# Kernel tuning notes

Measured on AMD Instinct MI355X. Metric: run time of the kernel, lower is better.

The kernel has to match this reference:

```python
import jax, jax.numpy as jnp
import numpy as np

D_MODEL = 1024
N_HEAD = 16
D_K = D_MODEL // N_HEAD
B, S = 2, 2048


def setup_inputs() -> dict:
    key = jax.random.key(0)
    ks = jax.random.split(key, 12)
    sc = 1.0 / np.sqrt(D_MODEL)
    return {
        "q": jax.random.normal(ks[0], (B, S, D_MODEL), jnp.float32),
        "k": jax.random.normal(ks[1], (B, S, D_MODEL), jnp.float32),
        "v": jax.random.normal(ks[2], (B, S, D_MODEL), jnp.float32),
        "mask": jax.random.randint(ks[3], (B, S, S), 0, 2, jnp.int32),
        # learned params (torch Linear convention: y = x @ W + b with W pre-transposed)
        "wq": jax.random.normal(ks[4], (D_MODEL, D_MODEL), jnp.float32) * sc,
        "bq": jax.random.normal(ks[5], (D_MODEL,), jnp.float32) * sc,
        "wk": jax.random.normal(ks[6], (D_MODEL, D_MODEL), jnp.float32) * sc,  # no bias
        "wv": jax.random.normal(ks[7], (D_MODEL, D_MODEL), jnp.float32) * sc,
        "bv": jax.random.normal(ks[8], (D_MODEL,), jnp.float32) * sc,
        "wf": jax.random.normal(ks[9], (D_MODEL, D_MODEL), jnp.float32) * sc,
        "bf": jax.random.normal(ks[10], (D_MODEL,), jnp.float32) * sc,
    }


def reference(q, k, v, mask, wq, bq, wk, wv, bv, wf, bf):
    bs = q.shape[0]
    temperature = jnp.asarray(D_K ** 0.5, q.dtype)
    # projections -> [b, h, s, d_k]
    qh = (q @ wq + bq).reshape(bs, -1, N_HEAD, D_K).transpose(0, 2, 1, 3)
    kh = (k @ wk).reshape(bs, -1, N_HEAD, D_K).transpose(0, 2, 1, 3)
    vh = (v @ wv + bv).reshape(bs, -1, N_HEAD, D_K).transpose(0, 2, 1, 3)
    # scores [b, h, sq, sk]
    attn = jnp.einsum("bhqd,bhkd->bhqk", qh, kh) / temperature
    m0 = (mask[:, None, :, :] == 0)  # mask==0 -> masked out, broadcast over heads
    attn = jnp.where(m0, -jnp.inf, attn)
    attn = jax.nn.softmax(attn, axis=-1)
    attn = jnp.where(m0, 0.0, attn)
    out = jnp.einsum("bhqk,bhkd->bhqd", attn, vh)
    out = out.transpose(0, 2, 1, 3).reshape(bs, -1, D_MODEL)
    return out @ wf + bf  # dropout is identity in eval mode
```

## Files before the change

### kernel.cpp

```cpp
#include <hip/hip_runtime.h>

#define D_MODEL 1024
#define NHEAD   16
#define DK      64
#define BATCH   2
#define SEQ     2048

typedef __attribute__((ext_vector_type(8))) short bf16x8;
typedef __attribute__((ext_vector_type(4))) short bf16x4;
typedef __attribute__((ext_vector_type(4))) float f32x4;
typedef __attribute__((ext_vector_type(2))) int i32x2;

#define QSCALE 0.18033688011f

__device__ __forceinline__ unsigned short f2b(float x) {
  unsigned u = __builtin_bit_cast(unsigned, x);
  u = (u + 0x7fffu + ((u >> 16) & 1u)) >> 16;
  return (unsigned short)u;
}
__device__ __forceinline__ unsigned short f2b_rhu(float x) {
  return (unsigned short)((__builtin_bit_cast(unsigned, x) + 0x8000u) >> 16);
}
__device__ __forceinline__ int pk2(float a, float b) {
  unsigned ua = __builtin_bit_cast(unsigned, a) + 0x8000u;
  unsigned ub = __builtin_bit_cast(unsigned, b) + 0x8000u;
  return (int)__builtin_amdgcn_perm(ub, ua, 0x07060302u);
}
__device__ __forceinline__ int pk2u(unsigned ua, unsigned ub) {
  return (int)__builtin_amdgcn_perm(ub + 0x8000u, ua + 0x8000u, 0x07060302u);
}

typedef const __attribute__((address_space(1))) void* gas_p;
typedef __attribute__((address_space(3))) void* las_p;
__device__ __forceinline__ void gll16(const void* g, void* l) {
  __builtin_amdgcn_global_load_lds((gas_p)g, (las_p)l, 16, 0, 0);
}

__device__ __forceinline__ f32x4 mfma16(bf16x4 a, bf16x4 b, f32x4 c) {
#if __has_builtin(__builtin_amdgcn_mfma_f32_16x16x16bf16_1k)
  return __builtin_amdgcn_mfma_f32_16x16x16bf16_1k(a, b, c, 0, 0, 0);
#else
  f32x4 d;
  asm("v_mfma_f32_16x16x16_bf16 %0, %1, %2, %3" : "=v"(d) : "v"(a), "v"(b), "v"(c));
  return d;
#endif
}

__global__ __launch_bounds__(256) void cast3_kernel(
    const float* __restrict__ q, const float* __restrict__ k, const float* __restrict__ v,
    unsigned short* __restrict__ qb, unsigned short* __restrict__ kb,
    unsigned short* __restrict__ vb) {
  const float* src = blockIdx.y == 0 ? q : (blockIdx.y == 1 ? k : v);
  unsigned short* dst = blockIdx.y == 0 ? qb : (blockIdx.y == 1 ? kb : vb);
  size_t i = ((size_t)blockIdx.x * 256 + threadIdx.x) * 8;
  float4 x0 = *(const float4*)&src[i];
  float4 x1 = *(const float4*)&src[i + 4];
  int4 w;
  w.x = pk2(x0.x, x0.y); w.y = pk2(x0.z, x0.w);
  w.z = pk2(x1.x, x1.y); w.w = pk2(x1.z, x1.w);
  *(int4*)&dst[i] = w;
}

__global__ __launch_bounds__(256) void wtrans_kernel(
    const float* __restrict__ wq, const float* __restrict__ wk,
    const float* __restrict__ wv, const float* __restrict__ wf,
    unsigned short* __restrict__ wqt, unsigned short* __restrict__ wkt,
    unsigned short* __restrict__ wvt, unsigned short* __restrict__ wft) {
  __shared__ float tile[64][65];
  const float* w; unsigned short* wt;
  switch (blockIdx.z) {
    case 0: w = wq; wt = wqt; break;
    case 1: w = wk; wt = wkt; break;
    case 2: w = wv; wt = wvt; break;
    default: w = wf; wt = wft; break;
  }
  int r0 = blockIdx.y * 64, c0 = blockIdx.x * 64;
  int t = threadIdx.x;
  for (int i = 0; i < 16; ++i) {
    int idx = t + i * 256; int r = idx >> 6, c = idx & 63;
    tile[r][c] = w[(size_t)(r0 + r) * D_MODEL + c0 + c];
  }
  __syncthreads();
  for (int i = 0; i < 16; ++i) {
    int idx = t + i * 256; int r = idx >> 6, c = idx & 63;
    wt[(size_t)(c0 + r) * D_MODEL + r0 + c] = f2b(tile[c][r]);
  }
}

__global__ __launch_bounds__(256) void maskpack_kernel(
    const int* __restrict__ mask, unsigned long long* __restrict__ mbits) {
  size_t gw = ((size_t)blockIdx.x * 256 + threadIdx.x) >> 6;
  int lane = threadIdx.x & 63;
  int val = mask[gw * 64 + lane];
  unsigned long long bits = __ballot(val != 0);
  if (lane == 0) mbits[gw] = bits;
}

__global__ __launch_bounds__(256) void gemm_qkv_kernel(
    const unsigned short* __restrict__ qb, const unsigned short* __restrict__ kb,
    const unsigned short* __restrict__ vb,
    const unsigned short* __restrict__ wqt, const unsigned short* __restrict__ wkt,
    const unsigned short* __restrict__ wvt,
    const float* __restrict__ bq, const float* __restrict__ bv,
    unsigned short* __restrict__ qh, unsigned short* __restrict__ kh,
    unsigned short* __restrict__ vt) {
  __shared__ unsigned short SB[16640];
  int bid = blockIdx.x;
  int xcd = bid & 7, slot = bid >> 3;
  int mi = slot & 3, zn = slot >> 2;
  int z = zn >> 3;
  int n0 = (zn & 7) * 128;
  int m0 = (mi * 8 + xcd) * 128;
  const unsigned short* A; const unsigned short* Bt;
  switch (z) {
    case 0:  A = qb; Bt = wqt; break;
    case 1:  A = kb; Bt = wkt; break;
    default: A = vb; Bt = wvt; break;
  }
  int t = threadIdx.x, lane = t & 63, wave = t >> 6;
  int l16 = lane & 15, quad = lane >> 4;
  int wm = (wave & 1) * 64, wn = (wave >> 1) * 64;
  f32x4 zero = {0.f, 0.f, 0.f, 0.f};
  f32x4 acc[4][4];
  for (int mt = 0; mt < 4; ++mt) for (int nt = 0; nt < 4; ++nt) acc[mt][nt] = zero;

  int drow = lane >> 2, dcol = (lane & 3) * 8;
  const unsigned short* asrc = A  + (size_t)(m0 + wave * 32 + drow) * D_MODEL + dcol;
  const unsigned short* bsrc = Bt + (size_t)(n0 + wave * 32 + drow) * D_MODEL + dcol;
  int dst = wave * 1024 + lane * 8;

#pragma unroll
  for (int g = 0; g < 2; ++g) {
    gll16(asrc + (size_t)(g * 16) * D_MODEL, &SB[dst + g * 512]);
    gll16(bsrc + (size_t)(g * 16) * D_MODEL, &SB[4096 + dst + g * 512]);
  }
  for (int it = 0; it < 32; ++it) {
    __syncthreads();
    if (it + 1 < 32) {
      int nb = ((it + 1) & 1) * 8192, kn = (it + 1) * 32;
#pragma unroll
      for (int g = 0; g < 2; ++g) {
        gll16(asrc + (size_t)(g * 16) * D_MODEL + kn, &SB[nb + dst + g * 512]);
        gll16(bsrc + (size_t)(g * 16) * D_MODEL + kn, &SB[nb + 4096 + dst + g * 512]);
      }
    }
    int cb = (it & 1) * 8192;
    bf16x8 a[4], b[4];
    for (int mt = 0; mt < 4; ++mt)
      a[mt] = *(const bf16x8*)&SB[cb + (wm + mt * 16 + l16) * 32 + quad * 8];
    for (int nt = 0; nt < 4; ++nt)
      b[nt] = *(const bf16x8*)&SB[cb + 4096 + (wn + nt * 16 + l16) * 32 + quad * 8];
    for (int mt = 0; mt < 4; ++mt)
      for (int nt = 0; nt < 4; ++nt)
        acc[mt][nt] = __builtin_amdgcn_mfma_f32_16x16x32_bf16(a[mt], b[nt], acc[mt][nt], 0, 0, 0);
  }

  if (z == 2) {
    __syncthreads();
#pragma unroll
    for (int nt = 0; nt < 4; ++nt) {
      int col = wn + nt * 16 + l16;
      float bb = bv[n0 + col];
      for (int mt = 0; mt < 4; ++mt)
        for (int r = 0; r < 4; ++r)
          SB[col * 130 + wm + mt * 16 + quad * 4 + r] = f2b_rhu(acc[mt][nt][r] + bb);
    }
    __syncthreads();
    int c = t >> 1, hf = t & 1;
    int colg = n0 + c, hh = colg >> 6, dd = colg & 63;
    int b_ = m0 >> 11, sbase = m0 & (SEQ - 1);
    unsigned short* dstp = vt + (((size_t)(b_ * NHEAD + hh)) * DK + dd) * SEQ + sbase + hf * 64;
#pragma unroll
    for (int j = 0; j < 8; ++j)
      *(int4*)(dstp + j * 8) = *(const int4*)&SB[c * 130 + hf * 64 + j * 8];
  } else if (z == 0) {
    for (int nt = 0; nt < 4; ++nt) {
      int col = n0 + wn + nt * 16 + l16;
      float bb = bq[col];
      int h = col >> 6, d = col & 63;
      for (int mt = 0; mt < 4; ++mt)
        for (int r = 0; r < 4; ++r) {
          int row = m0 + wm + mt * 16 + quad * 4 + r;
          int b_ = row >> 11, s = row & (SEQ - 1);
          qh[(((size_t)(b_ * NHEAD + h) * SEQ) + s) * DK + d] =
              f2b_rhu((acc[mt][nt][r] + bb) * QSCALE);
        }
    }
  } else {
    for (int nt = 0; nt < 4; ++nt) {
      int col = n0 + wn + nt * 16 + l16;
      int h = col >> 6, d = col & 63;
      for (int mt = 0; mt < 4; ++mt)
        for (int r = 0; r < 4; ++r) {
          int row = m0 + wm + mt * 16 + quad * 4 + r;
          int b_ = row >> 11, s = row & (SEQ - 1);
          kh[(((size_t)(b_ * NHEAD + h) * SEQ) + s) * DK + d] = f2b_rhu(acc[mt][nt][r]);
        }
    }
  }
}

__global__ __launch_bounds__(256) void gemm_out_kernel(
    const unsigned short* __restrict__ A, const unsigned short* __restrict__ Bt,
    const float* __restrict__ bias, float* __restrict__ out) {
  __shared__ unsigned short As[8192], Bs[8192];
  int bid = blockIdx.x;
  int xcd = bid & 7, slot = bid >> 3;
  int mi = slot & 7, n0 = (slot >> 3) * 64;
  int m0 = (mi * 8 + xcd) * 64;
  int t = threadIdx.x, lane = t & 63, wave = t >> 6;
  int l16 = lane & 15, quad = lane >> 4;
  int wm = (wave & 1) * 32, wn = (wave >> 1) * 32;
  f32x4 zero = {0.f, 0.f, 0.f, 0.f};
  f32x4 acc[2][2];
  for (int mt = 0; mt < 2; ++mt) for (int nt = 0; nt < 2; ++nt) acc[mt][nt] = zero;

  int drow = lane >> 2, dcol = (lane & 3) * 8;
  const unsigned short* asrc = A  + (size_t)(m0 + wave * 16 + drow) * D_MODEL + dcol;
  const unsigned short* bsrc = Bt + (size_t)(n0 + wave * 16 + drow) * D_MODEL + dcol;
  int dst = wave * 512 + lane * 8;

#pragma unroll
  for (int hf = 0; hf < 2; ++hf) {
    gll16(asrc + hf * 32, &As[dst + hf * 2048]);
    gll16(bsrc + hf * 32, &Bs[dst + hf * 2048]);
  }
  for (int it = 0; it < 16; ++it) {
    __syncthreads();
    if (it + 1 < 16) {
      int nb = ((it + 1) & 1) * 4096, kn = (it + 1) * 64;
#pragma unroll
      for (int hf = 0; hf < 2; ++hf) {
        gll16(asrc + kn + hf * 32, &As[nb + dst + hf * 2048]);
        gll16(bsrc + kn + hf * 32, &Bs[nb + dst + hf * 2048]);
      }
    }
    int cb = (it & 1) * 4096;
#pragma unroll
    for (int half = 0; half < 2; ++half) {
      bf16x8 a[2], b[2];
      for (int mt = 0; mt < 2; ++mt)
        a[mt] = *(const bf16x8*)&As[cb + half * 2048 + (wm + mt * 16 + l16) * 32 + quad * 8];
      for (int nt = 0; nt < 2; ++nt)
        b[nt] = *(const bf16x8*)&Bs[cb + half * 2048 + (wn + nt * 16 + l16) * 32 + quad * 8];
      for (int mt = 0; mt < 2; ++mt)
        for (int nt = 0; nt < 2; ++nt)
          acc[mt][nt] = __builtin_amdgcn_mfma_f32_16x16x32_bf16(a[mt], b[nt], acc[mt][nt], 0, 0, 0);
    }
  }
  for (int nt = 0; nt < 2; ++nt) {
    int col = n0 + wn + nt * 16 + l16;
    float bb = bias[col];
    for (int mt = 0; mt < 2; ++mt)
      for (int r = 0; r < 4; ++r) {
        int row = m0 + wm + mt * 16 + quad * 4 + r;
        out[(size_t)row * D_MODEL + col] = acc[mt][nt][r] + bb;
      }
  }
}

__global__ __launch_bounds__(256, 2) void attn_kernel(
    const unsigned short* __restrict__ qh, const unsigned short* __restrict__ kh,
    const unsigned short* __restrict__ vt, const unsigned long long* __restrict__ mbits,
    unsigned short* __restrict__ attb) {
  __shared__ unsigned short Ks[8192];
  __shared__ unsigned short Vs[8192];
  int bid = blockIdx.x;
  int xcd = bid & 7, slot = bid >> 3;
  int bh_ = 4 * xcd + (slot >> 4);
  int qt = slot & 15;
  int b = bh_ >> 4, h = bh_ & 15;
  int t = threadIdx.x, lane = t & 63, wave = t >> 6;
  int l16 = lane & 15, quad = lane >> 4;
  size_t bh = (size_t)b * NHEAD + h;

  const unsigned short* Kg = kh + bh * SEQ * DK;
  const unsigned short* Vg = vt + bh * DK * SEQ;
  const unsigned long long* mrow = mbits + (size_t)b * SEQ * (SEQ / 64);

  bf16x8 qf[2][2];
#pragma unroll
  for (int qm = 0; qm < 2; ++qm) {
    const unsigned short* Qg =
        qh + (bh * SEQ + (size_t)(qt * 128 + wave * 32 + qm * 16 + l16)) * DK;
    qf[qm][0] = *(const bf16x8*)&Qg[quad * 8];
    qf[qm][1] = *(const bf16x8*)&Qg[32 + quad * 8];
  }

  int srow = lane >> 3;
  int schk = ((lane & 7) ^ (srow & 7)) * 8;
  const unsigned short* ks0 = Kg + (size_t)(wave * 16 + srow) * DK + schk;
  const unsigned short* ks1 = Kg + (size_t)(wave * 16 + 8 + srow) * DK + schk;
  const unsigned short* vs0 = Vg + (size_t)(wave * 16 + srow) * SEQ + schk;
  const unsigned short* vs1 = Vg + (size_t)(wave * 16 + 8 + srow) * SEQ + schk;
  int sdst = wave * 1024 + lane * 8;

  int x7 = l16 & 7;
  int ka0 = l16 * 64 + ((quad ^ x7) * 8);
  int ka1 = l16 * 64 + (((4 + quad) ^ x7) * 8);
  int va[4];
#pragma unroll
  for (int nt = 0; nt < 4; ++nt)
    va[nt] = l16 * 64 + (((nt * 2 + (quad >> 1)) ^ x7) * 8) + (quad & 1) * 4;

  bf16x4 ones4;
#pragma unroll
  for (int i = 0; i < 4; ++i) ones4[i] = (short)0x3F80;

  f32x4 zero = {0.f, 0.f, 0.f, 0.f};
  f32x4 accO[2][4], accRS[2];
#pragma unroll
  for (int qm = 0; qm < 2; ++qm) {
    accRS[qm] = zero;
    for (int dt = 0; dt < 4; ++dt) accO[qm][dt] = zero;
  }

  gll16(ks0, &Ks[sdst]);       gll16(ks1, &Ks[sdst + 512]);
  gll16(vs0, &Vs[sdst]);       gll16(vs1, &Vs[sdst + 512]);

  for (int tk = 0; tk < SEQ / 64; ++tk) {
    __syncthreads();
    if (tk + 1 < SEQ / 64) {
      int nb = ((tk + 1) & 1) * 4096;
      size_t ko = (size_t)(tk + 1) * 64 * DK;
      int vo = (tk + 1) * 64;
      gll16(ks0 + ko, &Ks[nb + sdst]);  gll16(ks1 + ko, &Ks[nb + sdst + 512]);
      gll16(vs0 + vo, &Vs[nb + sdst]);  gll16(vs1 + vo, &Vs[nb + sdst + 512]);
    }
    int cb = (tk & 1) * 4096;

    f32x4 accS[2][4];
#pragma unroll
    for (int qm = 0; qm < 2; ++qm)
      for (int nt = 0; nt < 4; ++nt) accS[qm][nt] = zero;
#pragma unroll
    for (int step = 0; step < 2; ++step) {
      int ka = step ? ka1 : ka0;
#pragma unroll
      for (int nt = 0; nt < 4; ++nt) {
        bf16x8 kf = *(const bf16x8*)&Ks[cb + ka + nt * 1024];
        accS[0][nt] = __builtin_amdgcn_mfma_f32_16x16x32_bf16(kf, qf[0][step], accS[0][nt], 0, 0, 0);
        accS[1][nt] = __builtin_amdgcn_mfma_f32_16x16x32_bf16(kf, qf[1][step], accS[1][nt], 0, 0, 0);
      }
    }

    bf16x4 ap[2][4];
#pragma unroll
    for (int qm = 0; qm < 2; ++qm) {
      int qrow = qt * 128 + wave * 32 + qm * 16 + l16;
      unsigned long long mq = mrow[(size_t)qrow * (SEQ / 64) + tk] >> (quad * 4);
      unsigned mlo = (unsigned)mq, mhi = (unsigned)(mq >> 32);
#pragma unroll
      for (int nt = 0; nt < 4; ++nt) {
        unsigned w = (nt < 2) ? mlo : mhi;
        unsigned pu[4];
#pragma unroll
        for (int r = 0; r < 4; ++r) {
          float pv = __builtin_amdgcn_exp2f(accS[qm][nt][r]);
          int msk = ((int)(w << (31 - ((nt & 1) * 16 + r)))) >> 31;
          pu[r] = __builtin_bit_cast(unsigned, pv) & (unsigned)msk;
        }
        i32x2 wv;
        wv[0] = pk2u(pu[0], pu[1]);
        wv[1] = pk2u(pu[2], pu[3]);
        ap[qm][nt] = __builtin_bit_cast(bf16x4, wv);
      }
#pragma unroll
      for (int nt = 0; nt < 4; ++nt)
        accRS[qm] = mfma16(ap[qm][nt], ones4, accRS[qm]);
    }

#pragma unroll
    for (int nt = 0; nt < 4; ++nt) {
      int vb_ = cb + va[nt];
#pragma unroll
      for (int dt = 0; dt < 4; ++dt) {
        bf16x4 vf = *(const bf16x4*)&Vs[vb_ + dt * 1024];
        accO[0][dt] = mfma16(ap[0][nt], vf, accO[0][dt]);
        accO[1][dt] = mfma16(ap[1][nt], vf, accO[1][dt]);
      }
    }
  }

#pragma unroll
  for (int qm = 0; qm < 2; ++qm)
    for (int r = 0; r < 4; ++r) {
      float sden = accRS[qm][r];
      float inv = sden > 0.f ? 1.f / sden : 0.f;
      int row = qt * 128 + wave * 32 + qm * 16 + quad * 4 + r;
      size_t ob = ((size_t)b * SEQ + row) * D_MODEL + (size_t)h * DK;
      for (int dt = 0; dt < 4; ++dt)
        attb[ob + dt * 16 + l16] = f2b_rhu(accO[qm][dt][r] * inv);
    }
}

extern "C" void kernel_launch(void* const* d_in, const int* in_sizes, int n_in,
                              void* d_out, int out_size, void* d_ws, size_t ws_size,
                              hipStream_t stream) {
  (void)in_sizes; (void)n_in; (void)out_size; (void)ws_size;
  const float* q    = (const float*)d_in[0];
  const float* k    = (const float*)d_in[1];
  const float* v    = (const float*)d_in[2];
  const int*   mask = (const int*)d_in[3];
  const float* wq   = (const float*)d_in[4];
  const float* bq   = (const float*)d_in[5];
  const float* wk   = (const float*)d_in[6];
  const float* wv   = (const float*)d_in[7];
  const float* bv   = (const float*)d_in[8];
  const float* wf   = (const float*)d_in[9];
  const float* bf   = (const float*)d_in[10];

  char* ws = (char*)d_ws;
  unsigned short* wft  = (unsigned short*)(ws + 0);
  unsigned short* wqt  = (unsigned short*)(ws + 2097152);
  unsigned short* wkt  = (unsigned short*)(ws + 4194304);
  unsigned short* wvt  = (unsigned short*)(ws + 6291456);
  unsigned short* attb = (unsigned short*)(ws + 2097152);
  unsigned short* qhp  = (unsigned short*)(ws + 10485760);
  unsigned short* khp  = (unsigned short*)(ws + 18874368);
  unsigned short* vtp  = (unsigned short*)(ws + 27262976);
  unsigned long long* mbits = (unsigned long long*)(ws + 35651584);
  unsigned short* vb   = (unsigned short*)(ws + 36700160);
  unsigned short* qb   = (unsigned short*)d_out;
  unsigned short* kb   = (unsigned short*)d_out + 4194304;

  hipLaunchKernelGGL(cast3_kernel, dim3(2048, 3), dim3(256), 0, stream, q, k, v, qb, kb, vb);
  hipLaunchKernelGGL(wtrans_kernel, dim3(16, 16, 4), dim3(256), 0, stream,
                     wq, wk, wv, wf, wqt, wkt, wvt, wft);
  hipLaunchKernelGGL(maskpack_kernel, dim3(32768), dim3(256), 0, stream, mask, mbits);
  hipLaunchKernelGGL(gemm_qkv_kernel, dim3(768), dim3(256), 0, stream,
                     qb, kb, vb, wqt, wkt, wvt, bq, bv, qhp, khp, vtp);
  hipLaunchKernelGGL(attn_kernel, dim3(512), dim3(256), 0, stream,
                     qhp, khp, vtp, mbits, attb);
  hipLaunchKernelGGL(gemm_out_kernel, dim3(1024), dim3(256), 0, stream,
                     attb, wft, bf, (float*)d_out);
}
```

Measured before the change: 280.3 us.

## Merge prep kernels, stage Q/K stores through LDS, shrink attention blocks

Folds the three preprocessing kernels (input cast, weight transpose, mask bit-packing) into one launch dispatched by block index, and mask packing now handles four 64-wide words per wave. The Q/K projection epilogue writes through shared memory so global stores become 16-byte coalesced rows instead of scattered 2-byte writes. The attention kernel moves to 128-thread blocks covering 64 query rows, doubling the grid to 1024 blocks, and each wave now loads four K/V chunks. Mask words are fetched early in the loop. The aims are fewer launches, better store coalescing and more attention parallelism, at the cost of less K/V tile reuse per block.

```diff
diff --git a/kernel.cpp b/kernel.cpp
--- a/kernel.cpp
+++ b/kernel.cpp
@@ -46,54 +46,61 @@
 #endif
 }
 
-__global__ __launch_bounds__(256) void cast3_kernel(
+__global__ __launch_bounds__(256) void prep_kernel(
     const float* __restrict__ q, const float* __restrict__ k, const float* __restrict__ v,
     unsigned short* __restrict__ qb, unsigned short* __restrict__ kb,
-    unsigned short* __restrict__ vb) {
-  const float* src = blockIdx.y == 0 ? q : (blockIdx.y == 1 ? k : v);
-  unsigned short* dst = blockIdx.y == 0 ? qb : (blockIdx.y == 1 ? kb : vb);
-  size_t i = ((size_t)blockIdx.x * 256 + threadIdx.x) * 8;
-  float4 x0 = *(const float4*)&src[i];
-  float4 x1 = *(const float4*)&src[i + 4];
-  int4 w;
-  w.x = pk2(x0.x, x0.y); w.y = pk2(x0.z, x0.w);
-  w.z = pk2(x1.x, x1.y); w.w = pk2(x1.z, x1.w);
-  *(int4*)&dst[i] = w;
-}
-
-__global__ __launch_bounds__(256) void wtrans_kernel(
+    unsigned short* __restrict__ vb,
     const float* __restrict__ wq, const float* __restrict__ wk,
     const float* __restrict__ wv, const float* __restrict__ wf,
     unsigned short* __restrict__ wqt, unsigned short* __restrict__ wkt,
-    unsigned short* __restrict__ wvt, unsigned short* __restrict__ wft) {
-  __shared__ float tile[64][65];
-  const float* w; unsigned short* wt;
-  switch (blockIdx.z) {
-    case 0: w = wq; wt = wqt; break;
-    case 1: w = wk; wt = wkt; break;
-    case 2: w = wv; wt = wvt; break;
-    default: w = wf; wt = wft; break;
-  }
-  int r0 = blockIdx.y * 64, c0 = blockIdx.x * 64;
-  int t = threadIdx.x;
-  for (int i = 0; i < 16; ++i) {
-    int idx = t + i * 256; int r = idx >> 6, c = idx & 63;
-    tile[r][c] = w[(size_t)(r0 + r) * D_MODEL + c0 + c];
-  }
-  __syncthreads();
-  for (int i = 0; i < 16; ++i) {
-    int idx = t + i * 256; int r = idx >> 6, c = idx & 63;
-    wt[(size_t)(c0 + r) * D_MODEL + r0 + c] = f2b(tile[c][r]);
-  }
-}
-
-__global__ __launch_bounds__(256) void maskpack_kernel(
+    unsigned short* __restrict__ wvt, unsigned short* __restrict__ wft,
     const int* __restrict__ mask, unsigned long long* __restrict__ mbits) {
-  size_t gw = ((size_t)blockIdx.x * 256 + threadIdx.x) >> 6;
-  int lane = threadIdx.x & 63;
-  int val = mask[gw * 64 + lane];
-  unsigned long long bits = __ballot(val != 0);
-  if (lane == 0) mbits[gw] = bits;
+  int bid = blockIdx.x, t = threadIdx.x;
+  if (bid < 6144) {
+    int by = bid >> 11, bx = bid & 2047;
+    const float* src = by == 0 ? q : (by == 1 ? k : v);
+    unsigned short* dst = by == 0 ? qb : (by == 1 ? kb : vb);
+    size_t i = ((size_t)bx * 256 + t) * 8;
+    float4 x0 = *(const float4*)&src[i];
+    float4 x1 = *(const float4*)&src[i + 4];
+    int4 w;
+    w.x = pk2(x0.x, x0.y); w.y = pk2(x0.z, x0.w);
+    w.z = pk2(x1.x, x1.y); w.w = pk2(x1.z, x1.w);
+    *(int4*)&dst[i] = w;
+  } else if (bid < 7168) {
+    __shared__ float tile[64][65];
+    int idx = bid - 6144;
+    int bz = idx >> 8, by = (idx >> 4) & 15, bx = idx & 15;
+    const float* w; unsigned short* wt;
+    switch (bz) {
+      case 0: w = wq; wt = wqt; break;
+      case 1: w = wk; wt = wkt; break;
+      case 2: w = wv; wt = wvt; break;
+      default: w = wf; wt = wft; break;
+    }
+    int r0 = by * 64, c0 = bx * 64;
+    for (int i = 0; i < 16; ++i) {
+      int idx2 = t + i * 256; int r = idx2 >> 6, c = idx2 & 63;
+      tile[r][c] = w[(size_t)(r0 + r) * D_MODEL + c0 + c];
+    }
+    __syncthreads();
+    for (int i = 0; i < 16; ++i) {
+      int idx2 = t + i * 256; int r = idx2 >> 6, c = idx2 & 63;
+      wt[(size_t)(c0 + r) * D_MODEL + r0 + c] = f2b(tile[c][r]);
+    }
+  } else {
+    int idx = bid - 7168;
+    int lane = t & 63, wave = t >> 6;
+    size_t base = ((size_t)idx * 4 + wave) * 256;
+    unsigned long long b0 = __ballot(mask[base + lane] != 0);
+    unsigned long long b1 = __ballot(mask[base + 64 + lane] != 0);
+    unsigned long long b2 = __ballot(mask[base + 128 + lane] != 0);
+    unsigned long long b3 = __ballot(mask[base + 192 + lane] != 0);
+    if (lane == 0) {
+      unsigned long long* p = &mbits[(size_t)idx * 16 + wave * 4];
+      p[0] = b0; p[1] = b1; p[2] = b2; p[3] = b3;
+    }
+  }
 }
 
 __global__ __launch_bounds__(256) void gemm_qkv_kernel(
@@ -173,29 +180,30 @@
 #pragma unroll
     for (int j = 0; j < 8; ++j)
       *(int4*)(dstp + j * 8) = *(const int4*)&SB[c * 130 + hf * 64 + j * 8];
-  } else if (z == 0) {
+  } else {
+    __syncthreads();
+#pragma unroll
     for (int nt = 0; nt < 4; ++nt) {
-      int col = n0 + wn + nt * 16 + l16;
-      float bb = bq[col];
-      int h = col >> 6, d = col & 63;
+      int lcol = wn + nt * 16 + l16;
+      float bb = (z == 0) ? bq[n0 + lcol] : 0.f;
       for (int mt = 0; mt < 4; ++mt)
         for (int r = 0; r < 4; ++r) {
-          int row = m0 + wm + mt * 16 + quad * 4 + r;
-          int b_ = row >> 11, s = row & (SEQ - 1);
-          qh[(((size_t)(b_ * NHEAD + h) * SEQ) + s) * DK + d] =
-              f2b_rhu((acc[mt][nt][r] + bb) * QSCALE);
+          float val = acc[mt][nt][r] + bb;
+          if (z == 0) val *= QSCALE;
+          SB[(wm + mt * 16 + quad * 4 + r) * 130 + lcol] = f2b_rhu(val);
         }
     }
-  } else {
-    for (int nt = 0; nt < 4; ++nt) {
-      int col = n0 + wn + nt * 16 + l16;
-      int h = col >> 6, d = col & 63;
-      for (int mt = 0; mt < 4; ++mt)
-        for (int r = 0; r < 4; ++r) {
-          int row = m0 + wm + mt * 16 + quad * 4 + r;
-          int b_ = row >> 11, s = row & (SEQ - 1);
-          kh[(((size_t)(b_ * NHEAD + h) * SEQ) + s) * DK + d] = f2b_rhu(acc[mt][nt][r]);
-        }
+    __syncthreads();
+    unsigned short* outp = (z == 0) ? qh : kh;
+    int b_ = m0 >> 11, sbase = m0 & (SEQ - 1);
+    int h0 = n0 >> 6, c = t & 7;
+#pragma unroll
+    for (int pass = 0; pass < 8; ++pass) {
+      int rp = pass * 32 + (t >> 3);
+      int srow = rp >> 1, part = rp & 1;
+      unsigned short* dstp = outp +
+          (((size_t)(b_ * NHEAD + h0 + part)) * SEQ + sbase + srow) * DK + c * 8;
+      *(int4*)dstp = *(const int4*)&SB[srow * 130 + part * 64 + c * 8];
     }
   }
 }
@@ -259,7 +267,7 @@
   }
 }
 
-__global__ __launch_bounds__(256, 2) void attn_kernel(
+__global__ __launch_bounds__(128, 2) void attn_kernel(
     const unsigned short* __restrict__ qh, const unsigned short* __restrict__ kh,
     const unsigned short* __restrict__ vt, const unsigned long long* __restrict__ mbits,
     unsigned short* __restrict__ attb) {
@@ -267,8 +275,8 @@
   __shared__ unsigned short Vs[8192];
   int bid = blockIdx.x;
   int xcd = bid & 7, slot = bid >> 3;
-  int bh_ = 4 * xcd + (slot >> 4);
-  int qt = slot & 15;
+  int bh_ = 4 * xcd + (slot >> 5);
+  int qt = slot & 31;
   int b = bh_ >> 4, h = bh_ & 15;
   int t = threadIdx.x, lane = t & 63, wave = t >> 6;
   int l16 = lane & 15, quad = lane >> 4;
@@ -277,23 +285,21 @@
   const unsigned short* Kg = kh + bh * SEQ * DK;
   const unsigned short* Vg = vt + bh * DK * SEQ;
   const unsigned long long* mrow = mbits + (size_t)b * SEQ * (SEQ / 64);
+  int qrowb = qt * 64 + wave * 32;
 
   bf16x8 qf[2][2];
 #pragma unroll
   for (int qm = 0; qm < 2; ++qm) {
-    const unsigned short* Qg =
-        qh + (bh * SEQ + (size_t)(qt * 128 + wave * 32 + qm * 16 + l16)) * DK;
+    const unsigned short* Qg = qh + (bh * SEQ + (size_t)(qrowb + qm * 16 + l16)) * DK;
     qf[qm][0] = *(const bf16x8*)&Qg[quad * 8];
     qf[qm][1] = *(const bf16x8*)&Qg[32 + quad * 8];
   }
 
-  int srow = lane >> 3;
-  int schk = ((lane & 7) ^ (srow & 7)) * 8;
-  const unsigned short* ks0 = Kg + (size_t)(wave * 16 + srow) * DK + schk;
-  const unsigned short* ks1 = Kg + (size_t)(wave * 16 + 8 + srow) * DK + schk;
-  const unsigned short* vs0 = Vg + (size_t)(wave * 16 + srow) * SEQ + schk;
-  const unsigned short* vs1 = Vg + (size_t)(wave * 16 + 8 + srow) * SEQ + schk;
-  int sdst = wave * 1024 + lane * 8;
+  int srow8 = t >> 3;
+  int schk = ((t & 7) ^ (srow8 & 7)) * 8;
+  const unsigned short* ksrc = Kg + (size_t)srow8 * DK + schk;
+  const unsigned short* vsrc = Vg + (size_t)srow8 * SEQ + schk;
+  int sdst = t * 8;
 
   int x7 = l16 & 7;
   int ka0 = l16 * 64 + ((quad ^ x7) * 8);
@@ -303,6 +309,9 @@
   for (int nt = 0; nt < 4; ++nt)
     va[nt] = l16 * 64 + (((nt * 2 + (quad >> 1)) ^ x7) * 8) + (quad & 1) * 4;
 
+  size_t mi0 = (size_t)(qrowb + l16) * (SEQ / 64);
+  size_t mi1 = (size_t)(qrowb + 16 + l16) * (SEQ / 64);
+
   bf16x4 ones4;
 #pragma unroll
   for (int i = 0; i < 4; ++i) ones4[i] = (short)0x3F80;
@@ -315,18 +324,27 @@
     for (int dt = 0; dt < 4; ++dt) accO[qm][dt] = zero;
   }
 
-  gll16(ks0, &Ks[sdst]);       gll16(ks1, &Ks[sdst + 512]);
-  gll16(vs0, &Vs[sdst]);       gll16(vs1, &Vs[sdst + 512]);
+#pragma unroll
+  for (int g = 0; g < 4; ++g) {
+    gll16(ksrc + (size_t)(g * 16) * DK, &Ks[g * 1024 + sdst]);
+    gll16(vsrc + (size_t)(g * 16) * SEQ, &Vs[g * 1024 + sdst]);
+  }
 
   for (int tk = 0; tk < SEQ / 64; ++tk) {
     __syncthreads();
     if (tk + 1 < SEQ / 64) {
       int nb = ((tk + 1) & 1) * 4096;
-      size_t ko = (size_t)(tk + 1) * 64 * DK;
-      int vo = (tk + 1) * 64;
-      gll16(ks0 + ko, &Ks[nb + sdst]);  gll16(ks1 + ko, &Ks[nb + sdst + 512]);
-      gll16(vs0 + vo, &Vs[nb + sdst]);  gll16(vs1 + vo, &Vs[nb + sdst + 512]);
-    }
+      const unsigned short* kn = ksrc + (size_t)((tk + 1) * 64) * DK;
+      const unsigned short* vn = vsrc + (tk + 1) * 64;
+#pragma unroll
+      for (int g = 0; g < 4; ++g) {
+        gll16(kn + (size_t)(g * 16) * DK, &Ks[nb + g * 1024 + sdst]);
+        gll16(vn + (size_t)(g * 16) * SEQ, &Vs[nb + g * 1024 + sdst]);
+      }
+    }
+    unsigned long long mq0 = mrow[mi0 + tk];
+    unsigned long long mq1 = mrow[mi1 + tk];
+
     int cb = (tk & 1) * 4096;
 
     f32x4 accS[2][4];
@@ -347,8 +365,7 @@
     bf16x4 ap[2][4];
 #pragma unroll
     for (int qm = 0; qm < 2; ++qm) {
-      int qrow = qt * 128 + wave * 32 + qm * 16 + l16;
-      unsigned long long mq = mrow[(size_t)qrow * (SEQ / 64) + tk] >> (quad * 4);
+      unsigned long long mq = (qm ? mq1 : mq0) >> (quad * 4);
       unsigned mlo = (unsigned)mq, mhi = (unsigned)(mq >> 32);
 #pragma unroll
       for (int nt = 0; nt < 4; ++nt) {
@@ -387,7 +404,7 @@
     for (int r = 0; r < 4; ++r) {
       float sden = accRS[qm][r];
       float inv = sden > 0.f ? 1.f / sden : 0.f;
-      int row = qt * 128 + wave * 32 + qm * 16 + quad * 4 + r;
+      int row = qrowb + qm * 16 + quad * 4 + r;
       size_t ob = ((size_t)b * SEQ + row) * D_MODEL + (size_t)h * DK;
       for (int dt = 0; dt < 4; ++dt)
         attb[ob + dt * 16 + l16] = f2b_rhu(accO[qm][dt][r] * inv);
@@ -424,13 +441,12 @@
   unsigned short* qb   = (unsigned short*)d_out;
   unsigned short* kb   = (unsigned short*)d_out + 4194304;
 
-  hipLaunchKernelGGL(cast3_kernel, dim3(2048, 3), dim3(256), 0, stream, q, k, v, qb, kb, vb);
-  hipLaunchKernelGGL(wtrans_kernel, dim3(16, 16, 4), dim3(256), 0, stream,
-                     wq, wk, wv, wf, wqt, wkt, wvt, wft);
-  hipLaunchKernelGGL(maskpack_kernel, dim3(32768), dim3(256), 0, stream, mask, mbits);
+  hipLaunchKernelGGL(prep_kernel, dim3(15360), dim3(256), 0, stream,
+                     q, k, v, qb, kb, vb,
+                     wq, wk, wv, wf, wqt, wkt, wvt, wft, mask, mbits);
   hipLaunchKernelGGL(gemm_qkv_kernel, dim3(768), dim3(256), 0, stream,
                      qb, kb, vb, wqt, wkt, wvt, bq, bv, qhp, khp, vtp);
-  hipLaunchKernelGGL(attn_kernel, dim3(512), dim3(256), 0, stream,
+  hipLaunchKernelGGL(attn_kernel, dim3(1024), dim3(128), 0, stream,
                      qhp, khp, vtp, mbits, attb);
   hipLaunchKernelGGL(gemm_out_kernel, dim3(1024), dim3(256), 0, stream,
                      attb, wft, bf, (float*)d_out);
```

Measured after the change: 268.0 us. -4.4%, faster.
